# Performance work log

Hardware: AMD Instinct MI355X
Metric: run time of the kernel (lower is better)

## Reference

```python
import jax, jax.numpy as jnp
import numpy as np

V, E, H, L = 10000, 512, 512, 3   # vocab, embed dim, hidden, num decoder layers
SOS, EOS = 1, 2


def setup_inputs() -> dict:
    key = jax.random.key(0)
    ks = jax.random.split(key, 16)
    N, To, Ti = 32, 64, 512
    s = 0.05
    inp = {
        'padded_input': jax.random.randint(ks[0], (N, To), 0, V),
        'encoder_padded_outputs': jax.random.normal(ks[1], (N, Ti, H), jnp.float32),
        'emb': jax.random.normal(ks[2], (V, E), jnp.float32) * s,
        # layer 0 LSTMCell: input = embed + encoder context (E + H)
        'W_ih0': jax.random.normal(ks[3], (4 * H, E + H), jnp.float32) * s,
        'W_hh0': jax.random.normal(ks[4], (4 * H, H), jnp.float32) * s,
        'b_ih0': jnp.zeros((4 * H,), jnp.float32),
        'b_hh0': jnp.zeros((4 * H,), jnp.float32),
        # layers 1..L-1 LSTMCells (stacked)
        'W_ih_r': jax.random.normal(ks[5], (L - 1, 4 * H, H), jnp.float32) * s,
        'W_hh_r': jax.random.normal(ks[6], (L - 1, 4 * H, H), jnp.float32) * s,
        'b_ih_r': jnp.zeros((L - 1, 4 * H), jnp.float32),
        'b_hh_r': jnp.zeros((L - 1, 4 * H), jnp.float32),
        # MLP: Linear(2H -> H), Tanh, Linear(H -> V)
        'W1': jax.random.normal(ks[7], (H, 2 * H), jnp.float32) * s,
        'b1': jnp.zeros((H,), jnp.float32),
        'W2': jax.random.normal(ks[8], (V, H), jnp.float32) * s,
        'b2': jnp.zeros((V,), jnp.float32),
    }
    return inp


def _lstm_cell(x, h, c, Wi, Wh, bi, bh):
    # torch.nn.LSTMCell gate order: i, f, g, o
    g = x @ Wi.T + h @ Wh.T + bi + bh
    i, f, gg, o = jnp.split(g, 4, axis=-1)
    c2 = jax.nn.sigmoid(f) * c + jax.nn.sigmoid(i) * jnp.tanh(gg)
    h2 = jax.nn.sigmoid(o) * jnp.tanh(c2)
    return h2, c2


def reference(padded_input, encoder_padded_outputs, emb,
              W_ih0, W_hh0, b_ih0, b_hh0,
              W_ih_r, W_hh_r, b_ih_r, b_hh_r,
              W1, b1, W2, b2):
    N, To = padded_input.shape
    sos = jnp.full((N, 1), SOS, padded_input.dtype)
    eos = jnp.full((N, 1), EOS, padded_input.dtype)
    ys_in = jnp.concatenate([sos, padded_input], axis=1)    # [N, T]
    ys_out = jnp.concatenate([padded_input, eos], axis=1)   # [N, T]
    xs = jnp.transpose(emb[ys_in], (1, 0, 2))               # [T, N, E]

    def step(carry, x_t):
        h, c, att_c = carry                                  # h,c: [L,N,H]; att_c: [N,H]
        rnn_in = jnp.concatenate([x_t, att_c], axis=1)       # [N, E+H]
        h0, c0 = _lstm_cell(rnn_in, h[0], c[0], W_ih0, W_hh0, b_ih0, b_hh0)
        hs, cs = [h0], [c0]
        for l in range(L - 1):
            hl, cl = _lstm_cell(hs[-1], h[l + 1], c[l + 1],
                                W_ih_r[l], W_hh_r[l], b_ih_r[l], b_hh_r[l])
            hs.append(hl); cs.append(cl)
        r = hs[-1]                                           # [N, H]
        scores = jnp.einsum('nh,nth->nt', r, encoder_padded_outputs)
        w = jax.nn.softmax(scores, axis=-1)
        att = jnp.einsum('nt,nth->nh', w, encoder_padded_outputs)
        mlp_in = jnp.concatenate([r, att], axis=1)           # [N, 2H]
        y = jnp.tanh(mlp_in @ W1.T + b1) @ W2.T + b2         # [N, V]
        return (jnp.stack(hs), jnp.stack(cs), att), y

    h0 = jnp.zeros((L, N, H), encoder_padded_outputs.dtype)
    c0 = jnp.zeros((L, N, H), encoder_padded_outputs.dtype)
    a0 = jnp.zeros((N, H), encoder_padded_outputs.dtype)
    _, ys = jax.lax.scan(step, (h0, c0, a0), xs)             # [T, N, V]
    y_all = jnp.transpose(ys, (1, 0, 2))                     # [N, T, V]

    logp = jax.nn.log_softmax(y_all, axis=-1)
    nll = -jnp.take_along_axis(logp, ys_out[..., None], axis=-1)[..., 0]
    ce_loss = nll.mean()
    return y_all, ce_loss
```

## Files before the change

kernel.cpp:

```cpp
#include <hip/hip_runtime.h>
#include <hip/hip_bf16.h>
#include <hip/hip_fp16.h>

#define NB 32
#define TO 64
#define TT 65
#define TI 512
#define VV 10000
#define HH 512
#define G4 2048
#define SOS_ID 1
#define EOS_ID 2
#define NBLK 256

typedef unsigned uvec4 __attribute__((ext_vector_type(4)));
typedef unsigned uvec2 __attribute__((ext_vector_type(2)));
typedef _Float16 h2v __attribute__((ext_vector_type(2)));

__device__ __forceinline__ float cload1(const float* p) {
    unsigned v = __hip_atomic_load((const unsigned*)p,
                                   __ATOMIC_RELAXED, __HIP_MEMORY_SCOPE_AGENT);
    return __uint_as_float(v);
}
__device__ __forceinline__ float2 cload2(const float* p) {
    unsigned long long v = __hip_atomic_load((const unsigned long long*)p,
                                             __ATOMIC_RELAXED, __HIP_MEMORY_SCOPE_AGENT);
    float2 r;
    r.x = __uint_as_float((unsigned)(v & 0xffffffffull));
    r.y = __uint_as_float((unsigned)(v >> 32));
    return r;
}
__device__ __forceinline__ void cstore(float* p, float v) {
    __hip_atomic_store((unsigned*)p, __float_as_uint(v),
                       __ATOMIC_RELAXED, __HIP_MEMORY_SCOPE_AGENT);
}

__device__ __forceinline__ void gbar(int* flags, int g, int s, int& epoch) {
    asm volatile("s_waitcnt vmcnt(0) lgkmcnt(0)" ::: "memory");
    __syncthreads();
    epoch++;
    int tid = threadIdx.x;
    if (tid == 0)
        __hip_atomic_store(&flags[(g * 32 + s) * 16], epoch,
                           __ATOMIC_RELAXED, __HIP_MEMORY_SCOPE_AGENT);
    if (tid < 32) {
        for (;;) {
            int v = __hip_atomic_load(&flags[(g * 32 + tid) * 16],
                                      __ATOMIC_RELAXED, __HIP_MEMORY_SCOPE_AGENT);
            unsigned long long b = __ballot(v >= epoch);
            if ((b & 0xffffffffull) == 0xffffffffull) break;
            __builtin_amdgcn_s_sleep(1);
        }
    }
    __syncthreads();
}

__device__ __forceinline__ float bf2f(unsigned u16) {
    return __uint_as_float(u16 << 16);
}
__device__ __forceinline__ unsigned f2bf(float f) {
    unsigned u = __float_as_uint(f);
    return (u + 0x7fffu + ((u >> 16) & 1u)) >> 16;
}
__device__ __forceinline__ unsigned packh2(float a, float b) {
    __half2 h = __floats2half2_rn(a, b);
    return *(unsigned*)&h;
}
__device__ __forceinline__ h2v uash2(unsigned u) {
    union { unsigned u; h2v h; } c; c.u = u; return c.h;
}

template <int KQ4>
__device__ __forceinline__ void lstm_phase(
    const unsigned* __restrict__ Wtb, const float* __restrict__ bi,
    const float* __restrict__ bh, float* __restrict__ hout,
    float& creg, float* __restrict__ mlprow,
    float4* xs4, float* sg, float* sg2, int s, int n0,
    const float* __restrict__ pre) {
    int tid = threadIdx.x;
    int lane = tid & 63, wv = tid >> 6;
    const uvec2* wp = (const uvec2*)Wtb + (long)(wv * KQ4) * 2048 + (s * 64 + lane);
    const float4* xp = (const float4*)xs4 + wv * KQ4 * 4;
    float a0 = 0.f, a1 = 0.f, a2 = 0.f, a3 = 0.f;
#pragma unroll 4
    for (int kq = 0; kq < KQ4; kq++) {
        uvec2 u = wp[(long)kq * 2048];
        float w0 = bf2f(u.x & 0xffffu), w1 = bf2f(u.x >> 16);
        float w2 = bf2f(u.y & 0xffffu), w3 = bf2f(u.y >> 16);
        float4 x0 = xp[4 * kq], x1 = xp[4 * kq + 1];
        float4 x2 = xp[4 * kq + 2], x3 = xp[4 * kq + 3];
        a0 = fmaf(w0, x0.x, a0); a1 = fmaf(w0, x0.y, a1);
        a2 = fmaf(w0, x0.z, a2); a3 = fmaf(w0, x0.w, a3);
        a0 = fmaf(w1, x1.x, a0); a1 = fmaf(w1, x1.y, a1);
        a2 = fmaf(w1, x1.z, a2); a3 = fmaf(w1, x1.w, a3);
        a0 = fmaf(w2, x2.x, a0); a1 = fmaf(w2, x2.y, a1);
        a2 = fmaf(w2, x2.z, a2); a3 = fmaf(w2, x2.w, a3);
        a0 = fmaf(w3, x3.x, a0); a1 = fmaf(w3, x3.y, a1);
        a2 = fmaf(w3, x3.z, a2); a3 = fmaf(w3, x3.w, a3);
    }
    float4 r4; r4.x = a0; r4.y = a1; r4.z = a2; r4.w = a3;
    ((float4*)sg)[wv * 64 + lane] = r4;
    __syncthreads();
    {
        int c = tid >> 4, n = (tid >> 2) & 3, w4 = tid & 3;
        float sum = sg[((w4 * 4 + 0) * 64 + c) * 4 + n]
                  + sg[((w4 * 4 + 1) * 64 + c) * 4 + n]
                  + sg[((w4 * 4 + 2) * 64 + c) * 4 + n]
                  + sg[((w4 * 4 + 3) * 64 + c) * 4 + n];
        sg2[tid] = sum;
    }
    __syncthreads();
    if (tid < 64) {
        int gn = tid >> 4, gml = tid & 15, gm = s * 16 + gml;
        float ga[4];
#pragma unroll
        for (int q = 0; q < 4; q++) {
            int c = q * 16 + gml;
            const float* p = sg2 + c * 16 + gn * 4;
            ga[q] = p[0] + p[1] + p[2] + p[3];
        }
        float gi = ga[0] + bi[gm] + bh[gm];
        float gf = ga[1] + bi[512 + gm] + bh[512 + gm];
        float gg = ga[2] + bi[1024 + gm] + bh[1024 + gm];
        float go = ga[3] + bi[1536 + gm] + bh[1536 + gm];
        float si = 1.f / (1.f + expf(-gi));
        float sf = 1.f / (1.f + expf(-gf));
        float so = 1.f / (1.f + expf(-go));
        float c2 = sf * creg + si * tanhf(gg);
        creg = c2;
        float hv = so * tanhf(c2);
        cstore(&hout[(n0 + gn) * 512 + gm], hv);
        if (mlprow) mlprow[(long)(n0 + gn) * 1024 + gm] = hv;
    } else if (pre && tid >= 512 && tid < 768) {
        int k = 512 + (tid - 512) * 2;
        float2 va = cload2(pre + (n0 + 0) * 512 + (k - 512));
        float2 vb = cload2(pre + (n0 + 1) * 512 + (k - 512));
        float2 vc = cload2(pre + (n0 + 2) * 512 + (k - 512));
        float2 vd = cload2(pre + (n0 + 3) * 512 + (k - 512));
        float4 x0, x1;
        x0.x = va.x; x0.y = vb.x; x0.z = vc.x; x0.w = vd.x;
        x1.x = va.y; x1.y = vb.y; x1.z = vc.y; x1.w = vd.y;
        xs4[k] = x0; xs4[k + 1] = x1;
    }
}

__global__ __launch_bounds__(1024, 4) void decode_loop(
    const unsigned* __restrict__ Wtb0, const unsigned* __restrict__ Wtb1,
    const unsigned* __restrict__ Wtb2, const float* __restrict__ emb,
    const int* __restrict__ tokens, const float* __restrict__ enc,
    const float* __restrict__ b_ih0, const float* __restrict__ b_hh0,
    const float* __restrict__ b_ih_r, const float* __restrict__ b_hh_r,
    float* __restrict__ hbuf, float* __restrict__ attc,
    float* __restrict__ scor, float* __restrict__ mlpin, int* flags) {
    __shared__ float4 xs4[1536];
    __shared__ float sg[4096];
    __shared__ float sg2[1024];
    __shared__ unsigned short enct[32768];
    float* xsf = (float*)xs4;

    int tid = threadIdx.x, b = blockIdx.x;
    int g = b >> 5, s = b & 31;
    int epoch = 0;
    int n0 = g * 4;
    int lane = tid & 63;
    int na = n0 + (s >> 3), tiq = s & 7;
    float c0r = 0.f, c1r = 0.f, c2r = 0.f;

    {
        int tl = tid >> 4;
        int gb = (tid & 15) * 4;
        const float* ebase = enc + ((long)na * TI + tiq * 64 + tl) * HH;
#pragma unroll
        for (int q = 0; q < 4; q++) {
            int gg = gb + q;
            const float* ep = ebase + gg * 8;
            float4 lo = *(const float4*)ep;
            float4 hi = *(const float4*)(ep + 4);
            uvec4 pk;
            pk.x = f2bf(lo.x) | (f2bf(lo.y) << 16);
            pk.y = f2bf(lo.z) | (f2bf(lo.w) << 16);
            pk.z = f2bf(hi.x) | (f2bf(hi.y) << 16);
            pk.w = f2bf(hi.z) | (f2bf(hi.w) << 16);
            *(uvec4*)(enct + tl * 512 + (gg ^ (tl & 7)) * 8) = pk;
        }
    }
    __syncthreads();

    for (int t = 0; t < TT; t++) {
        int rp = t & 1;
        float* hOld = hbuf + rp * 3 * NB * HH;
        float* hNew = hbuf + (rp ^ 1) * 3 * NB * HH;
        float* h0r = hOld;
        float* h1r = hOld + NB * HH;
        float* h2r = hOld + 2 * NB * HH;
        float* h0w = hNew;
        float* h1w = hNew + NB * HH;
        float* h2w = hNew + 2 * NB * HH;

        if (t == 0) {
            if (tid < 768) {
                int k = tid * 2;
                float2 va, vb, vc, vd;
                if (k < 512) {
                    va = *(const float2*)(emb + (long)SOS_ID * 512 + k);
                    vb = va; vc = va; vd = va;
                } else if (k < 1024) {
                    va.x = va.y = 0.f; vb = va; vc = va; vd = va;
                } else {
                    int kk = k - 1024;
                    va = cload2(h0r + (n0 + 0) * 512 + kk);
                    vb = cload2(h0r + (n0 + 1) * 512 + kk);
                    vc = cload2(h0r + (n0 + 2) * 512 + kk);
                    vd = cload2(h0r + (n0 + 3) * 512 + kk);
                }
                float4 x0, x1;
                x0.x = va.x; x0.y = vb.x; x0.z = vc.x; x0.w = vd.x;
                x1.x = va.y; x1.y = vb.y; x1.z = vc.y; x1.w = vd.y;
                xs4[k] = x0; xs4[k + 1] = x1;
            }
        } else {
            if (tid < 256) {
                int kk = tid * 2;
                float2 va = cload2(attc + (n0 + 0) * 512 + kk);
                float2 vb = cload2(attc + (n0 + 1) * 512 + kk);
                float2 vc = cload2(attc + (n0 + 2) * 512 + kk);
                float2 vd = cload2(attc + (n0 + 3) * 512 + kk);
                if ((kk >> 4) == s) {
                    float* mp = mlpin + ((long)(t - 1) * NB + n0) * 1024 + 512 + kk;
                    mp[0] = va.x; mp[1] = va.y;
                    mp[1024] = vb.x; mp[1025] = vb.y;
                    mp[2048] = vc.x; mp[2049] = vc.y;
                    mp[3072] = vd.x; mp[3073] = vd.y;
                }
                float4 x0, x1;
                x0.x = va.x; x0.y = vb.x; x0.z = vc.x; x0.w = vd.x;
                x1.x = va.y; x1.y = vb.y; x1.z = vc.y; x1.w = vd.y;
                xs4[512 + kk] = x0; xs4[512 + kk + 1] = x1;
            }
        }
        __syncthreads();
        lstm_phase<24>(Wtb0, b_ih0, b_hh0, h0w, c0r, nullptr,
                       xs4, sg, sg2, s, n0, h1r);
        gbar(flags, g, s, epoch);

        if (tid < 64) cstore(&attc[n0 * 512 + s * 64 + tid], 0.f);
        if (tid < 256) {
            int k = tid * 2;
            float2 va = cload2(h0w + (n0 + 0) * 512 + k);
            float2 vb = cload2(h0w + (n0 + 1) * 512 + k);
            float2 vc = cload2(h0w + (n0 + 2) * 512 + k);
            float2 vd = cload2(h0w + (n0 + 3) * 512 + k);
            float4 x0, x1;
            x0.x = va.x; x0.y = vb.x; x0.z = vc.x; x0.w = vd.x;
            x1.x = va.y; x1.y = vb.y; x1.z = vc.y; x1.w = vd.y;
            xs4[k] = x0; xs4[k + 1] = x1;
        }
        __syncthreads();
        lstm_phase<16>(Wtb1, b_ih_r, b_hh_r, h1w, c1r, nullptr,
                       xs4, sg, sg2, s, n0, h2r);
        gbar(flags, g, s, epoch);

        if (tid < 256) {
            int k = tid * 2;
            float2 va = cload2(h1w + (n0 + 0) * 512 + k);
            float2 vb = cload2(h1w + (n0 + 1) * 512 + k);
            float2 vc = cload2(h1w + (n0 + 2) * 512 + k);
            float2 vd = cload2(h1w + (n0 + 3) * 512 + k);
            float4 x0, x1;
            x0.x = va.x; x0.y = vb.x; x0.z = vc.x; x0.w = vd.x;
            x1.x = va.y; x1.y = vb.y; x1.z = vc.y; x1.w = vd.y;
            xs4[k] = x0; xs4[k + 1] = x1;
        }
        __syncthreads();
        lstm_phase<16>(Wtb2, b_ih_r + G4, b_hh_r + G4, h2w, c2r,
                       mlpin + (long)t * NB * 1024,
                       xs4, sg, sg2, s, n0, nullptr);
        gbar(flags, g, s, epoch);

        if (tid < 512) xsf[tid] = cload1(h2w + na * 512 + tid);
        __syncthreads();
        {
            int tl = tid & 63, kh = tid >> 6;
            float acc = 0.f;
#pragma unroll
            for (int q = 0; q < 4; q++) {
                int gg = kh * 4 + q;
                uvec4 e = *(const uvec4*)(enct + tl * 512 + ((gg ^ (tl & 7)) * 8));
                const float* hp = xsf + gg * 8;
                acc += bf2f(e.x & 0xffffu) * hp[0] + bf2f(e.x >> 16) * hp[1]
                     + bf2f(e.y & 0xffffu) * hp[2] + bf2f(e.y >> 16) * hp[3]
                     + bf2f(e.z & 0xffffu) * hp[4] + bf2f(e.z >> 16) * hp[5]
                     + bf2f(e.w & 0xffffu) * hp[6] + bf2f(e.w >> 16) * hp[7];
            }
            sg[tid] = acc;
            __syncthreads();
            if (tid < 64) {
                float sv = 0.f;
#pragma unroll
                for (int w = 0; w < 16; w++) sv += sg[tid + 64 * w];
                cstore(&scor[na * 512 + tiq * 64 + tid], sv);
            }
        }
        gbar(flags, g, s, epoch);

        {
            float sv = (tid < 512) ? cload1(scor + na * 512 + tid) : -1e30f;
            int wv = tid >> 6;
            float m = sv;
#pragma unroll
            for (int o = 32; o > 0; o >>= 1) m = fmaxf(m, __shfl_xor(m, o));
            if (lane == 0) sg[wv] = m;
            __syncthreads();
            m = sg[0];
#pragma unroll
            for (int w = 1; w < 16; w++) m = fmaxf(m, sg[w]);
            float e = expf(sv - m);
            float ss = e;
#pragma unroll
            for (int o = 32; o > 0; o >>= 1) ss += __shfl_xor(ss, o);
            if (lane == 0) sg[32 + wv] = ss;
            __syncthreads();
            float tot = 0.f;
#pragma unroll
            for (int w = 0; w < 16; w++) tot += sg[32 + w];
            float inv = 1.f / tot;
            __syncthreads();
            if (tid < 512) sg[64 + tid] = e * inv;
            __syncthreads();

            int hp = (tid & 255) * 2, tis = (tid >> 8) * 16;
            int gb2 = hp >> 3, wrd = hp & 7;
            const float* wrow = sg + 64 + tiq * 64;
            float a0 = 0.f, a1 = 0.f;
#pragma unroll 8
            for (int q = 0; q < 16; q++) {
                int tl = tis + q;
                unsigned u = *(const unsigned*)(enct + tl * 512 +
                                                ((gb2 ^ (tl & 7)) * 8) + wrd);
                float w = wrow[tl];
                a0 = fmaf(w, bf2f(u & 0xffffu), a0);
                a1 = fmaf(w, bf2f(u >> 16), a1);
            }
            float* prt = sg + 1024;
            prt[(tid >> 8) * 512 + hp] = a0;
            prt[(tid >> 8) * 512 + hp + 1] = a1;
            __syncthreads();
            if (tid < 512) {
                int h = tid;
                float v = prt[h] + prt[512 + h] + prt[1024 + h] + prt[1536 + h];
                atomicAdd(&attc[na * 512 + h], v);
            }
            if (t + 1 < TT) {
                if (tid < 512) {
                    int k = tid;
                    int r0 = tokens[(n0 + 0) * TO + t];
                    int r1 = tokens[(n0 + 1) * TO + t];
                    int r2 = tokens[(n0 + 2) * TO + t];
                    int r3 = tokens[(n0 + 3) * TO + t];
                    float4 v;
                    v.x = emb[(long)r0 * 512 + k];
                    v.y = emb[(long)r1 * 512 + k];
                    v.z = emb[(long)r2 * 512 + k];
                    v.w = emb[(long)r3 * 512 + k];
                    xs4[k] = v;
                } else {
                    int k = tid - 512;
                    float4 v;
                    v.x = cload1(h0w + (n0 + 0) * 512 + k);
                    v.y = cload1(h0w + (n0 + 1) * 512 + k);
                    v.z = cload1(h0w + (n0 + 2) * 512 + k);
                    v.w = cload1(h0w + (n0 + 3) * 512 + k);
                    xs4[1024 + k] = v;
                }
            }
        }
        gbar(flags, g, s, epoch);
    }

    if (tid < 64) {
        int h = tiq * 64 + tid;
        mlpin[((long)(TT - 1) * NB + na) * 1024 + 512 + h] =
            cload1(attc + na * 512 + h);
    }
}

__global__ void transpose_lstm_q(const float* __restrict__ Wih, int KA,
                                 const float* __restrict__ Whh,
                                 unsigned* __restrict__ Wtb) {
    int K = KA + 512;
    long total = (long)(K / 4) * 4096;
    for (long idx = (long)blockIdx.x * 256 + threadIdx.x; idx < total;
         idx += (long)gridDim.x * 256) {
        int c2 = (int)(idx % 4096);
        int kq = (int)(idx / 4096);
        int c = c2 >> 1, half = c2 & 1;
        int sI = c >> 6, r = c & 63, gg = r >> 4, ml = r & 15;
        int j = gg * 512 + sI * 16 + ml;
        int k0 = kq * 4 + half * 2, k1 = k0 + 1;
        float w0 = (k0 < KA) ? Wih[(long)j * KA + k0] : Whh[(long)j * 512 + (k0 - KA)];
        float w1 = (k1 < KA) ? Wih[(long)j * KA + k1] : Whh[(long)j * 512 + (k1 - KA)];
        Wtb[idx] = f2bf(w0) | (f2bf(w1) << 16);
    }
}

__global__ void transpose_w2_h2(const float* __restrict__ W2,
                                unsigned* __restrict__ Wh) {
    long total = (long)256 * 10240;
    for (long idx = (long)blockIdx.x * 256 + threadIdx.x; idx < total;
         idx += (long)gridDim.x * 256) {
        int j = (int)(idx % 10240);
        int kk = (int)(idx / 10240);
        float lo = 0.f, hi = 0.f;
        if (j < VV) {
            lo = W2[(long)j * 512 + 2 * kk];
            hi = W2[(long)j * 512 + 2 * kk + 1];
        }
        Wh[idx] = packh2(lo, hi);
    }
}

__global__ void transpose_cat(const float* __restrict__ A, int KA,
                              int J, int Jp, float* __restrict__ Wt) {
    long total = (long)KA * Jp;
    for (long idx = (long)blockIdx.x * 256 + threadIdx.x; idx < total;
         idx += (long)gridDim.x * 256) {
        int j = (int)(idx % Jp);
        int k = (int)(idx / Jp);
        Wt[idx] = (j < J) ? A[(long)j * KA + k] : 0.f;
    }
}

__global__ void gemm_mlp1(const float* __restrict__ Wt,
                          const float* __restrict__ X,
                          const float* __restrict__ bias,
                          unsigned* __restrict__ outh) {
    __shared__ float xs[64 * 12];
    int m0 = blockIdx.x * 8;
    int lane = threadIdx.x & 63;
    int wv = threadIdx.x >> 6;
    int jp = wv * 64 + lane;
    float acc0[8], acc1[8];
#pragma unroll
    for (int q = 0; q < 8; q++) { acc0[q] = 0.f; acc1[q] = 0.f; }
    for (int kc = 0; kc < 1024; kc += 64) {
        __syncthreads();
        for (int idx = threadIdx.x; idx < 512; idx += 256) {
            int k = idx >> 3, n = idx & 7;
            xs[k * 12 + n] = X[(long)(m0 + n) * 1024 + kc + k];
        }
        __syncthreads();
        const float2* wpp = (const float2*)(Wt + (long)kc * 512) + jp;
#pragma unroll 4
        for (int k = 0; k < 64; k++) {
            float2 w = wpp[(long)k * 256];
            const float4* xv = (const float4*)(xs + k * 12);
            float4 x0 = xv[0], x1 = xv[1];
            acc0[0] += w.x * x0.x; acc0[1] += w.x * x0.y;
            acc0[2] += w.x * x0.z; acc0[3] += w.x * x0.w;
            acc0[4] += w.x * x1.x; acc0[5] += w.x * x1.y;
            acc0[6] += w.x * x1.z; acc0[7] += w.x * x1.w;
            acc1[0] += w.y * x0.x; acc1[1] += w.y * x0.y;
            acc1[2] += w.y * x0.z; acc1[3] += w.y * x0.w;
            acc1[4] += w.y * x1.x; acc1[5] += w.y * x1.y;
            acc1[6] += w.y * x1.z; acc1[7] += w.y * x1.w;
        }
    }
    float b0 = bias[2 * jp], b1 = bias[2 * jp + 1];
#pragma unroll
    for (int n = 0; n < 8; n++) {
        float v0 = tanhf(acc0[n] + b0);
        float v1 = tanhf(acc1[n] + b1);
        outh[(long)(m0 + n) * 256 + jp] = packh2(v0, v1);
    }
}

__global__ void gemm_mlp2(const unsigned* __restrict__ Wh,
                          const unsigned* __restrict__ Xh,
                          const float* __restrict__ bias,
                          float* __restrict__ out) {
    __shared__ unsigned xs[256 * 36];
    int t = blockIdx.y;
    int m0 = t * 32;
    int lane = threadIdx.x & 63;
    int wv = threadIdx.x >> 6;
    int j0 = blockIdx.x * 256 + wv * 64 + lane;
    float acc0[32], acc1[32];
#pragma unroll
    for (int q = 0; q < 32; q++) { acc0[q] = 0.f; acc1[q] = 0.f; }
    for (int idx = threadIdx.x; idx < 8192; idx += 256) {
        int kk = idx & 255, n = idx >> 8;
        xs[kk * 36 + n] = Xh[(long)(m0 + n) * 256 + kk];
    }
    __syncthreads();
    const unsigned* wpp = Wh + j0;
#pragma unroll 2
    for (int kk = 0; kk < 256; kk++) {
        unsigned u0 = wpp[(long)kk * 10240];
        unsigned u1 = wpp[(long)kk * 10240 + 5120];
        h2v w0 = uash2(u0), w1 = uash2(u1);
        const uvec4* xv = (const uvec4*)(xs + kk * 36);
#pragma unroll
        for (int q = 0; q < 8; q++) {
            uvec4 x4 = xv[q];
            acc0[4 * q + 0] = __builtin_amdgcn_fdot2(uash2(x4.x), w0, acc0[4 * q + 0], false);
            acc0[4 * q + 1] = __builtin_amdgcn_fdot2(uash2(x4.y), w0, acc0[4 * q + 1], false);
            acc0[4 * q + 2] = __builtin_amdgcn_fdot2(uash2(x4.z), w0, acc0[4 * q + 2], false);
            acc0[4 * q + 3] = __builtin_amdgcn_fdot2(uash2(x4.w), w0, acc0[4 * q + 3], false);
            acc1[4 * q + 0] = __builtin_amdgcn_fdot2(uash2(x4.x), w1, acc1[4 * q + 0], false);
            acc1[4 * q + 1] = __builtin_amdgcn_fdot2(uash2(x4.y), w1, acc1[4 * q + 1], false);
            acc1[4 * q + 2] = __builtin_amdgcn_fdot2(uash2(x4.z), w1, acc1[4 * q + 2], false);
            acc1[4 * q + 3] = __builtin_amdgcn_fdot2(uash2(x4.w), w1, acc1[4 * q + 3], false);
        }
    }
#pragma unroll
    for (int nn = 0; nn < 32; nn++) {
        long row = (long)nn * TT + t;
        float* po = out + row * VV;
        int ja = j0, jb = j0 + 5120;
        po[ja] = acc0[nn] + bias[ja];
        if (jb < VV) po[jb] = acc1[nn] + bias[jb];
    }
}

__global__ void loss_rows(const float* __restrict__ out, const int* __restrict__ tokens,
                          float* __restrict__ nll) {
    __shared__ float red[256];
    int row = blockIdx.x;
    int n = row / TT, t = row % TT;
    const float* y = out + (long)row * VV;
    int tid = threadIdx.x;
    float m = -1e30f;
    for (int v = tid; v < VV; v += 256) m = fmaxf(m, y[v]);
    red[tid] = m;
    __syncthreads();
    for (int s = 128; s > 0; s >>= 1) {
        if (tid < s) red[tid] = fmaxf(red[tid], red[tid + s]);
        __syncthreads();
    }
    m = red[0];
    __syncthreads();
    float sum = 0.f;
    for (int v = tid; v < VV; v += 256) sum += expf(y[v] - m);
    red[tid] = sum;
    __syncthreads();
    for (int s = 128; s > 0; s >>= 1) {
        if (tid < s) red[tid] += red[tid + s];
        __syncthreads();
    }
    if (tid == 0) {
        int target = (t < TO) ? tokens[n * TO + t] : EOS_ID;
        nll[row] = m + logf(red[0]) - y[target];
    }
}

__global__ void loss_final(const float* __restrict__ nll, float* __restrict__ out_loss) {
    __shared__ float red[256];
    int tid = threadIdx.x;
    float s = 0.f;
    for (int i = tid; i < NB * TT; i += 256) s += nll[i];
    red[tid] = s;
    __syncthreads();
    for (int k = 128; k > 0; k >>= 1) {
        if (tid < k) red[tid] += red[tid + k];
        __syncthreads();
    }
    if (tid == 0) *out_loss = red[0] / (float)(NB * TT);
}

extern "C" void kernel_launch(void* const* d_in, const int* in_sizes, int n_in,
                              void* d_out, int out_size, void* d_ws, size_t ws_size,
                              hipStream_t stream) {
    const int* padded   = (const int*)d_in[0];
    const float* enc    = (const float*)d_in[1];
    const float* emb    = (const float*)d_in[2];
    const float* W_ih0  = (const float*)d_in[3];
    const float* W_hh0  = (const float*)d_in[4];
    const float* b_ih0  = (const float*)d_in[5];
    const float* b_hh0  = (const float*)d_in[6];
    const float* W_ih_r = (const float*)d_in[7];
    const float* W_hh_r = (const float*)d_in[8];
    const float* b_ih_r = (const float*)d_in[9];
    const float* b_hh_r = (const float*)d_in[10];
    const float* W1     = (const float*)d_in[11];
    const float* b1     = (const float*)d_in[12];
    const float* W2     = (const float*)d_in[13];
    const float* b2     = (const float*)d_in[14];
    float* out = (float*)d_out;
    float* ws  = (float*)d_ws;

    unsigned* Wtb0 = (unsigned*)ws;
    unsigned* Wtb1 = Wtb0 + 384 * 4096;
    unsigned* Wtb2 = Wtb1 + 256 * 4096;
    unsigned* Wh   = Wtb2 + 256 * 4096;
    float* Wm1  = (float*)(Wh + 256 * 10240);
    float* hbuf = Wm1 + 1024 * 512;
    float* attc = hbuf + 2 * 3 * NB * HH;
    float* scor = attc + NB * HH;
    float* mlpin= scor + NB * TI;
    unsigned* y1h = (unsigned*)(mlpin + (long)TT * NB * 1024);
    float* nll  = (float*)(y1h + (long)TT * NB * 256);
    int*   flags= (int*)(nll + 2080);

    hipMemsetAsync(hbuf, 0, (size_t)(2 * 3 * NB * HH + 2 * NB * HH) * sizeof(float), stream);
    hipMemsetAsync(flags, 0, 8 * 32 * 16 * sizeof(int), stream);

    transpose_cat<<<1024, 256, 0, stream>>>(W1, 1024, 512, 512, Wm1);
    transpose_lstm_q<<<2048, 256, 0, stream>>>(W_ih0, 1024, W_hh0, Wtb0);
    transpose_lstm_q<<<2048, 256, 0, stream>>>(W_ih_r, 512, W_hh_r, Wtb1);
    transpose_lstm_q<<<2048, 256, 0, stream>>>(W_ih_r + 2048 * 512, 512,
                                               W_hh_r + 2048 * 512, Wtb2);
    transpose_w2_h2<<<2048, 256, 0, stream>>>(W2, Wh);

    decode_loop<<<NBLK, 1024, 0, stream>>>(Wtb0, Wtb1, Wtb2, emb, padded, enc,
                                           b_ih0, b_hh0, b_ih_r, b_hh_r,
                                           hbuf, attc, scor, mlpin, flags);

    gemm_mlp1<<<260, 256, 0, stream>>>(Wm1, mlpin, b1, y1h);
    gemm_mlp2<<<dim3(20, TT), 256, 0, stream>>>(Wh, y1h, b2, out);
    loss_rows<<<NB * TT, 256, 0, stream>>>(out, padded, nll);
    loss_final<<<1, 256, 0, stream>>>(nll, out + (long)NB * TT * VV);
}
```

Measured before the change: 2.330 ms.

## Use split softmax partials for attention to remove a grid barrier per step

Each block now computes a local max and sum-of-exp over its 64-position slice of attention scores and writes unnormalized partial context vectors. The next step merges the eight partials with a log-sum-exp rescale. This removes the global score exchange, one inter-block barrier per timestep, and the atomicAdd accumulation with its zeroing. In exchange the merge reads all eight partial vectors at the start of each step and adds some exp work. The final step gets the same merge.

```diff
diff --git a/kernel.cpp b/kernel.cpp
--- a/kernel.cpp
+++ b/kernel.cpp
@@ -150,19 +150,18 @@
     const int* __restrict__ tokens, const float* __restrict__ enc,
     const float* __restrict__ b_ih0, const float* __restrict__ b_hh0,
     const float* __restrict__ b_ih_r, const float* __restrict__ b_hh_r,
-    float* __restrict__ hbuf, float* __restrict__ attc,
-    float* __restrict__ scor, float* __restrict__ mlpin, int* flags) {
+    float* __restrict__ hbuf, float* __restrict__ pvec, float* __restrict__ pm,
+    float* __restrict__ mlpin, int* flags) {
     __shared__ float4 xs4[1536];
     __shared__ float sg[4096];
     __shared__ float sg2[1024];
+    __shared__ float wl[64];
     __shared__ unsigned short enct[32768];
-    float* xsf = (float*)xs4;
 
     int tid = threadIdx.x, b = blockIdx.x;
     int g = b >> 5, s = b & 31;
     int epoch = 0;
     int n0 = g * 4;
-    int lane = tid & 63;
     int na = n0 + (s >> 3), tiq = s & 7;
     float c0r = 0.f, c1r = 0.f, c2r = 0.f;
 
@@ -218,32 +217,63 @@
                 x1.x = va.y; x1.y = vb.y; x1.z = vc.y; x1.w = vd.y;
                 xs4[k] = x0; xs4[k + 1] = x1;
             }
+            __syncthreads();
         } else {
+            if (tid < 32) {
+                int nn = tid >> 3, bb = tid & 7;
+                sg[tid * 2] = cload1(&pm[((n0 + nn) * 8 + bb) * 2]);
+                sg[tid * 2 + 1] = cload1(&pm[((n0 + nn) * 8 + bb) * 2 + 1]);
+            }
+            __syncthreads();
+            {
+                int nn = tid >> 8, hp = (tid & 255) * 2;
+                float M = -1e30f;
+#pragma unroll
+                for (int bb = 0; bb < 8; bb++) M = fmaxf(M, sg[(nn * 8 + bb) * 2]);
+                float al[8];
+                float den = 0.f;
+#pragma unroll
+                for (int bb = 0; bb < 8; bb++) {
+                    al[bb] = expf(sg[(nn * 8 + bb) * 2] - M);
+                    den += al[bb] * sg[(nn * 8 + bb) * 2 + 1];
+                }
+                float inv = 1.f / den;
+                float a0 = 0.f, a1 = 0.f;
+#pragma unroll
+                for (int bb = 0; bb < 8; bb++) {
+                    float c = al[bb] * inv;
+                    float2 v = cload2(&pvec[((long)(n0 + nn) * 8 + bb) * 512 + hp]);
+                    a0 = fmaf(c, v.x, a0);
+                    a1 = fmaf(c, v.y, a1);
+                }
+                sg[1024 + nn * 512 + hp] = a0;
+                sg[1024 + nn * 512 + hp + 1] = a1;
+            }
+            __syncthreads();
             if (tid < 256) {
                 int kk = tid * 2;
-                float2 va = cload2(attc + (n0 + 0) * 512 + kk);
-                float2 vb = cload2(attc + (n0 + 1) * 512 + kk);
-                float2 vc = cload2(attc + (n0 + 2) * 512 + kk);
-                float2 vd = cload2(attc + (n0 + 3) * 512 + kk);
+                float v0a = sg[1024 + 0 * 512 + kk], v0b = sg[1024 + 0 * 512 + kk + 1];
+                float v1a = sg[1024 + 1 * 512 + kk], v1b = sg[1024 + 1 * 512 + kk + 1];
+                float v2a = sg[1024 + 2 * 512 + kk], v2b = sg[1024 + 2 * 512 + kk + 1];
+                float v3a = sg[1024 + 3 * 512 + kk], v3b = sg[1024 + 3 * 512 + kk + 1];
                 if ((kk >> 4) == s) {
                     float* mp = mlpin + ((long)(t - 1) * NB + n0) * 1024 + 512 + kk;
-                    mp[0] = va.x; mp[1] = va.y;
-                    mp[1024] = vb.x; mp[1025] = vb.y;
-                    mp[2048] = vc.x; mp[2049] = vc.y;
-                    mp[3072] = vd.x; mp[3073] = vd.y;
+                    mp[0] = v0a; mp[1] = v0b;
+                    mp[1024] = v1a; mp[1025] = v1b;
+                    mp[2048] = v2a; mp[2049] = v2b;
+                    mp[3072] = v3a; mp[3073] = v3b;
                 }
                 float4 x0, x1;
-                x0.x = va.x; x0.y = vb.x; x0.z = vc.x; x0.w = vd.x;
-                x1.x = va.y; x1.y = vb.y; x1.z = vc.y; x1.w = vd.y;
+                x0.x = v0a; x0.y = v1a; x0.z = v2a; x0.w = v3a;
+                x1.x = v0b; x1.y = v1b; x1.z = v2b; x1.w = v3b;
                 xs4[512 + kk] = x0; xs4[512 + kk + 1] = x1;
             }
-        }
-        __syncthreads();
+            __syncthreads();
+        }
         lstm_phase<24>(Wtb0, b_ih0, b_hh0, h0w, c0r, nullptr,
                        xs4, sg, sg2, s, n0, h1r);
         gbar(flags, g, s, epoch);
 
-        if (tid < 64) cstore(&attc[n0 * 512 + s * 64 + tid], 0.f);
         if (tid < 256) {
             int k = tid * 2;
             float2 va = cload2(h0w + (n0 + 0) * 512 + k);
@@ -277,7 +307,7 @@
                        xs4, sg, sg2, s, n0, nullptr);
         gbar(flags, g, s, epoch);
 
-        if (tid < 512) xsf[tid] = cload1(h2w + na * 512 + tid);
+        if (tid < 512) sg2[tid] = cload1(h2w + na * 512 + tid);
         __syncthreads();
         {
             int tl = tid & 63, kh = tid >> 6;
@@ -286,58 +316,43 @@
             for (int q = 0; q < 4; q++) {
                 int gg = kh * 4 + q;
                 uvec4 e = *(const uvec4*)(enct + tl * 512 + ((gg ^ (tl & 7)) * 8));
-                const float* hp = xsf + gg * 8;
+                const float* hp = sg2 + gg * 8;
                 acc += bf2f(e.x & 0xffffu) * hp[0] + bf2f(e.x >> 16) * hp[1]
                      + bf2f(e.y & 0xffffu) * hp[2] + bf2f(e.y >> 16) * hp[3]
                      + bf2f(e.z & 0xffffu) * hp[4] + bf2f(e.z >> 16) * hp[5]
                      + bf2f(e.w & 0xffffu) * hp[6] + bf2f(e.w >> 16) * hp[7];
             }
             sg[tid] = acc;
-            __syncthreads();
-            if (tid < 64) {
-                float sv = 0.f;
-#pragma unroll
-                for (int w = 0; w < 16; w++) sv += sg[tid + 64 * w];
-                cstore(&scor[na * 512 + tiq * 64 + tid], sv);
-            }
-        }
-        gbar(flags, g, s, epoch);
-
+        }
+        __syncthreads();
+        if (tid < 64) {
+            float sv = 0.f;
+#pragma unroll
+            for (int w = 0; w < 16; w++) sv += sg[tid + 64 * w];
+            float mb = sv;
+#pragma unroll
+            for (int o = 32; o > 0; o >>= 1) mb = fmaxf(mb, __shfl_xor(mb, o));
+            float e = expf(sv - mb);
+            float db = e;
+#pragma unroll
+            for (int o = 32; o > 0; o >>= 1) db += __shfl_xor(db, o);
+            wl[tid] = e;
+            if (tid == 0) {
+                cstore(&pm[(na * 8 + tiq) * 2], mb);
+                cstore(&pm[(na * 8 + tiq) * 2 + 1], db);
+            }
+        }
+        __syncthreads();
         {
-            float sv = (tid < 512) ? cload1(scor + na * 512 + tid) : -1e30f;
-            int wv = tid >> 6;
-            float m = sv;
-#pragma unroll
-            for (int o = 32; o > 0; o >>= 1) m = fmaxf(m, __shfl_xor(m, o));
-            if (lane == 0) sg[wv] = m;
-            __syncthreads();
-            m = sg[0];
-#pragma unroll
-            for (int w = 1; w < 16; w++) m = fmaxf(m, sg[w]);
-            float e = expf(sv - m);
-            float ss = e;
-#pragma unroll
-            for (int o = 32; o > 0; o >>= 1) ss += __shfl_xor(ss, o);
-            if (lane == 0) sg[32 + wv] = ss;
-            __syncthreads();
-            float tot = 0.f;
-#pragma unroll
-            for (int w = 0; w < 16; w++) tot += sg[32 + w];
-            float inv = 1.f / tot;
-            __syncthreads();
-            if (tid < 512) sg[64 + tid] = e * inv;
-            __syncthreads();
-
             int hp = (tid & 255) * 2, tis = (tid >> 8) * 16;
             int gb2 = hp >> 3, wrd = hp & 7;
-            const float* wrow = sg + 64 + tiq * 64;
             float a0 = 0.f, a1 = 0.f;
 #pragma unroll 8
             for (int q = 0; q < 16; q++) {
                 int tl = tis + q;
                 unsigned u = *(const unsigned*)(enct + tl * 512 +
                                                 ((gb2 ^ (tl & 7)) * 8) + wrd);
-                float w = wrow[tl];
+                float w = wl[tl];
                 a0 = fmaf(w, bf2f(u & 0xffffu), a0);
                 a1 = fmaf(w, bf2f(u >> 16), a1);
             }
@@ -348,7 +363,7 @@
             if (tid < 512) {
                 int h = tid;
                 float v = prt[h] + prt[512 + h] + prt[1024 + h] + prt[1536 + h];
-                atomicAdd(&attc[na * 512 + h], v);
+                cstore(&pvec[((long)na * 8 + tiq) * 512 + h], v);
             }
             if (t + 1 < TT) {
                 if (tid < 512) {
@@ -379,8 +394,23 @@
 
     if (tid < 64) {
         int h = tiq * 64 + tid;
-        mlpin[((long)(TT - 1) * NB + na) * 1024 + 512 + h] =
-            cload1(attc + na * 512 + h);
+        float mm[8], dd[8], al[8];
+        float M = -1e30f;
+#pragma unroll
+        for (int bb = 0; bb < 8; bb++) {
+            mm[bb] = cload1(&pm[(na * 8 + bb) * 2]);
+            dd[bb] = cload1(&pm[(na * 8 + bb) * 2 + 1]);
+            M = fmaxf(M, mm[bb]);
+        }
+        float den = 0.f;
+#pragma unroll
+        for (int bb = 0; bb < 8; bb++) { al[bb] = expf(mm[bb] - M); den += al[bb] * dd[bb]; }
+        float inv = 1.f / den;
+        float v = 0.f;
+#pragma unroll
+        for (int bb = 0; bb < 8; bb++)
+            v += (al[bb] * inv) * cload1(&pvec[((long)na * 8 + bb) * 512 + h]);
+        mlpin[((long)(TT - 1) * NB + na) * 1024 + 512 + h] = v;
     }
 }
 
@@ -594,14 +624,14 @@
     unsigned* Wh   = Wtb2 + 256 * 4096;
     float* Wm1  = (float*)(Wh + 256 * 10240);
     float* hbuf = Wm1 + 1024 * 512;
-    float* attc = hbuf + 2 * 3 * NB * HH;
-    float* scor = attc + NB * HH;
-    float* mlpin= scor + NB * TI;
+    float* mlpin= hbuf + 2 * 3 * NB * HH;
     unsigned* y1h = (unsigned*)(mlpin + (long)TT * NB * 1024);
-    float* nll  = (float*)(y1h + (long)TT * NB * 256);
+    float* pvec = (float*)(y1h + (long)TT * NB * 256);
+    float* pm   = pvec + 32 * 8 * 512;
+    float* nll  = pm + 512;
     int*   flags= (int*)(nll + 2080);
 
-    hipMemsetAsync(hbuf, 0, (size_t)(2 * 3 * NB * HH + 2 * NB * HH) * sizeof(float), stream);
+    hipMemsetAsync(hbuf, 0, (size_t)(2 * 3 * NB * HH) * sizeof(float), stream);
     hipMemsetAsync(flags, 0, 8 * 32 * 16 * sizeof(int), stream);
 
     transpose_cat<<<1024, 256, 0, stream>>>(W1, 1024, 512, 512, Wm1);
@@ -613,7 +643,7 @@
 
     decode_loop<<<NBLK, 1024, 0, stream>>>(Wtb0, Wtb1, Wtb2, emb, padded, enc,
                                            b_ih0, b_hh0, b_ih_r, b_hh_r,
-                                           hbuf, attc, scor, mlpin, flags);
+                                           hbuf, pvec, pm, mlpin, flags);
 
     gemm_mlp1<<<260, 256, 0, stream>>>(Wm1, mlpin, b1, y1h);
     gemm_mlp2<<<dim3(20, TT), 256, 0, stream>>>(Wh, y1h, b2, out);
```

After: 2.218 ms. -4.8%, faster.
